# Optimization experiments

Measured on AMD Instinct MI355X. Metric: run time of the kernel, lower is better.

Reference implementation:

```python
import jax, jax.numpy as jnp
import numpy as np

N_TOKENS = 8192
EMBED = 1024
HIDDEN = 4 * EMBED
NUM_EXPERTS = 8


def setup_inputs() -> dict:
    key = jax.random.key(0)
    ks = jax.random.split(key, 10)
    s = 0.02
    return {
        "x": jax.random.normal(ks[0], (N_TOKENS, EMBED), dtype=jnp.float32),
        # Router params
        "Wr1": jax.random.normal(ks[1], (EMBED, EMBED), dtype=jnp.float32) * s,
        "br1": jnp.zeros((EMBED,), dtype=jnp.float32),
        "Wr2": jax.random.normal(ks[2], (EMBED, NUM_EXPERTS), dtype=jnp.float32) * s,
        "br2": jnp.zeros((NUM_EXPERTS,), dtype=jnp.float32),
        # Expert FFN params, stacked over experts
        "W1": jax.random.normal(ks[3], (NUM_EXPERTS, EMBED, HIDDEN), dtype=jnp.float32) * s,
        "b1": jnp.zeros((NUM_EXPERTS, HIDDEN), dtype=jnp.float32),
        "W2": jax.random.normal(ks[4], (NUM_EXPERTS, HIDDEN, EMBED), dtype=jnp.float32) * s,
        "b2": jnp.zeros((NUM_EXPERTS, EMBED), dtype=jnp.float32),
    }


def reference(x, Wr1, br1, Wr2, br2, W1, b1, W2, b2):
    # Router: Linear -> ReLU -> Linear -> softmax over experts -> top-1
    h = jax.nn.relu(x @ Wr1 + br1)                      # [N, E]
    probs = jax.nn.softmax(h @ Wr2 + br2, axis=1)       # [N, num_experts]
    chosen = jnp.argmax(probs, axis=1)                  # [N]

    num_experts = W1.shape[0]
    out = jnp.zeros_like(x)
    # Fixed small loop over experts (structurally distinct weights).
    for e in range(num_experts):
        ffn_e = jax.nn.relu(x @ W1[e] + b1[e]) @ W2[e] + b2[e]  # [N, E]
        out = jnp.where((chosen == e)[:, None], ffn_e, out)
    # Note: original returns raw expert output (no probability weighting).
    return out
```

## Files before the change

kernel.cpp:

```cpp
#include <hip/hip_runtime.h>
#include <stdint.h>

#define N_TOK 8192
#define EMB 1024
#define HID 4096
#define NEXP 8

typedef _Float16 f16x8 __attribute__((ext_vector_type(8)));
typedef _Float16 f16x4 __attribute__((ext_vector_type(4)));
typedef short    s16x8 __attribute__((ext_vector_type(8)));
typedef unsigned short u16x8 __attribute__((ext_vector_type(8)));
typedef float    f32x4 __attribute__((ext_vector_type(4)));

typedef __attribute__((address_space(1))) const void gvoid_t;
typedef __attribute__((address_space(3))) void lvoid_t;

__device__ __forceinline__ void async16(const void* g, void* l) {
  __builtin_amdgcn_global_load_lds((gvoid_t*)g, (lvoid_t*)l, 16, 0, 0);
}

__device__ __forceinline__ unsigned short f2bf(float f) {
  unsigned u = __builtin_bit_cast(unsigned, f);
  u += 0x7fffu + ((u >> 16) & 1u);
  return (unsigned short)(u >> 16);
}

__global__ __launch_bounds__(256) void k_cast_x(const float* __restrict__ x,
    unsigned short* __restrict__ xb, _Float16* __restrict__ xhi, _Float16* __restrict__ xlo) {
  int i = (blockIdx.x * 256 + threadIdx.x) << 2;
  float4 v = *(const float4*)(x + i);
  ushort4 b;
  b.x = f2bf(v.x); b.y = f2bf(v.y); b.z = f2bf(v.z); b.w = f2bf(v.w);
  *(ushort4*)(xb + i) = b;
  float vv[4] = {v.x, v.y, v.z, v.w};
  f16x4 hi, lo;
#pragma unroll
  for (int j = 0; j < 4; j++) {
    _Float16 h = (_Float16)vv[j];
    hi[j] = h;
    lo[j] = (_Float16)(vv[j] - (float)h);
  }
  *(f16x4*)(xhi + i) = hi;
  *(f16x4*)(xlo + i) = lo;
}

__global__ __launch_bounds__(256) void k_trans_wr1(const float* __restrict__ src,
    _Float16* __restrict__ dhi, _Float16* __restrict__ dlo) {
  int nblk = blockIdx.x >> 4, kc = blockIdx.x & 15;
  int n = (nblk << 8) + threadIdx.x;
  int k0 = kc << 6;
  for (int k = k0; k < k0 + 64; k += 8) {
    f16x8 hi, lo;
#pragma unroll
    for (int j = 0; j < 8; j++) {
      float w = src[(size_t)(k + j) * EMB + n] * 256.0f;
      _Float16 h = (_Float16)w;
      hi[j] = h;
      lo[j] = (_Float16)(w - (float)h);
    }
    *(f16x8*)(dhi + (size_t)n * EMB + k) = hi;
    *(f16x8*)(dlo + (size_t)n * EMB + k) = lo;
  }
}

__global__ __launch_bounds__(256) void k_transcast_v2(const float* __restrict__ src,
    unsigned short* __restrict__ dst, int K, int Nn, int ktiles, int ntiles) {
  __shared__ __align__(16) unsigned short lds[256 * 72];
  int b = blockIdx.x;
  int e = b / (ktiles * ntiles);
  int r = b % (ktiles * ntiles);
  int kt = r / ntiles, nt = r % ntiles;
  int k0 = kt << 6, n0 = nt << 8;
  const float* s = src + (size_t)e * K * Nn;
  unsigned short* d = dst + (size_t)e * K * Nn;
  int tid = threadIdx.x;
  const float* scol = s + n0 + tid;
#pragma unroll 4
  for (int k = 0; k < 64; k += 2) {
    float a  = scol[(size_t)(k0 + k) * Nn];
    float bv = scol[(size_t)(k0 + k + 1) * Nn];
    unsigned p = (unsigned)f2bf(a) | ((unsigned)f2bf(bv) << 16);
    *(unsigned*)(lds + tid * 72 + k) = p;
  }
  __syncthreads();
  int c = tid & 7, nl = tid >> 3;
#pragma unroll
  for (int p2 = 0; p2 < 8; p2++) {
    int n = (p2 << 5) + nl;
    u16x8 v = *(const u16x8*)(lds + n * 72 + (c << 3));
    *(u16x8*)(d + (size_t)(n0 + n) * K + k0 + (c << 3)) = v;
  }
}

__global__ __launch_bounds__(256) void k_router_gemm(
    const _Float16* __restrict__ Ah, const _Float16* __restrict__ Al,
    const _Float16* __restrict__ Bh, const _Float16* __restrict__ Bl,
    const float* __restrict__ br1, float* __restrict__ hOut) {
  __shared__ __align__(16) _Float16 sAh[4096], sAl[4096], sBh[4096], sBl[4096];
  const int tid = threadIdx.x, lane = tid & 63, wave = tid >> 6;
  const int m0 = (blockIdx.x >> 3) << 7;
  const int n0 = (blockIdx.x & 7) << 7;
  const int srow = (wave << 5) + (lane >> 2);
  const int scol = (lane & 3) << 3;
  const size_t aBase = (size_t)(m0 + srow) * EMB + scol;
  const size_t bBase = (size_t)(n0 + srow) * EMB + scol;
  _Float16* lAh = sAh + (wave << 10);
  _Float16* lAl = sAl + (wave << 10);
  _Float16* lBh = sBh + (wave << 10);
  _Float16* lBl = sBl + (wave << 10);
  const int q = lane >> 4, c = lane & 15;
  const int msub = (wave & 1) << 6, nsub = (wave >> 1) << 6;
  f32x4 acc[4][4];
#pragma unroll
  for (int i = 0; i < 4; i++)
#pragma unroll
    for (int j = 0; j < 4; j++) acc[i][j] = (f32x4){0.f, 0.f, 0.f, 0.f};

  for (int kk = 0; kk < EMB; kk += 32) {
    async16(Ah + aBase + kk, lAh);
    async16(Ah + aBase + 16 * EMB + kk, lAh + 512);
    async16(Al + aBase + kk, lAl);
    async16(Al + aBase + 16 * EMB + kk, lAl + 512);
    async16(Bh + bBase + kk, lBh);
    async16(Bh + bBase + 16 * EMB + kk, lBh + 512);
    async16(Bl + bBase + kk, lBl);
    async16(Bl + bBase + 16 * EMB + kk, lBl + 512);
    __syncthreads();
    f16x8 fah[4], fal[4], fbh[4], fbl[4];
#pragma unroll
    for (int i = 0; i < 4; i++) {
      int ar = msub + (i << 4) + c;
      int br = nsub + (i << 4) + c;
      fah[i] = *(const f16x8*)(sAh + (ar << 5) + (q << 3));
      fal[i] = *(const f16x8*)(sAl + (ar << 5) + (q << 3));
      fbh[i] = *(const f16x8*)(sBh + (br << 5) + (q << 3));
      fbl[i] = *(const f16x8*)(sBl + (br << 5) + (q << 3));
    }
#pragma unroll
    for (int mi = 0; mi < 4; mi++)
#pragma unroll
      for (int ni = 0; ni < 4; ni++) {
        acc[mi][ni] = __builtin_amdgcn_mfma_f32_16x16x32_f16(fah[mi], fbh[ni], acc[mi][ni], 0, 0, 0);
        acc[mi][ni] = __builtin_amdgcn_mfma_f32_16x16x32_f16(fah[mi], fbl[ni], acc[mi][ni], 0, 0, 0);
        acc[mi][ni] = __builtin_amdgcn_mfma_f32_16x16x32_f16(fal[mi], fbh[ni], acc[mi][ni], 0, 0, 0);
      }
    __syncthreads();
  }
#pragma unroll
  for (int mi = 0; mi < 4; mi++)
#pragma unroll
    for (int ni = 0; ni < 4; ni++) {
      int gn = n0 + nsub + (ni << 4) + c;
      float bias = 256.0f * br1[gn];
#pragma unroll
      for (int i2 = 0; i2 < 4; i2++) {
        int gm = m0 + msub + (mi << 4) + (q << 2) + i2;
        float v = acc[mi][ni][i2] + bias;
        hOut[(size_t)gm * EMB + gn] = v > 0.f ? v : 0.f;
      }
    }
}

__global__ __launch_bounds__(256) void k_logits(const float* __restrict__ h,
    const float* __restrict__ Wr2, const float* __restrict__ br2, int* __restrict__ chosen) {
  __shared__ __align__(16) float sW[EMB * NEXP];
  int tid = threadIdx.x;
  for (int i = tid; i < EMB * NEXP; i += 256) sW[i] = Wr2[i];
  __syncthreads();
  int lane = tid & 63, wave = tid >> 6;
  int t = blockIdx.x * 4 + wave;
  const float* hr = h + (size_t)t * EMB;
  float acc[8] = {0.f, 0.f, 0.f, 0.f, 0.f, 0.f, 0.f, 0.f};
#pragma unroll
  for (int i = 0; i < 16; i++) {
    int k = (i << 6) + lane;
    float v = hr[k];
    float4 w0 = *(const float4*)(sW + (k << 3));
    float4 w1 = *(const float4*)(sW + (k << 3) + 4);
    acc[0] += v * w0.x; acc[1] += v * w0.y; acc[2] += v * w0.z; acc[3] += v * w0.w;
    acc[4] += v * w1.x; acc[5] += v * w1.y; acc[6] += v * w1.z; acc[7] += v * w1.w;
  }
#pragma unroll
  for (int off = 32; off > 0; off >>= 1)
#pragma unroll
    for (int e = 0; e < 8; e++) acc[e] += __shfl_down(acc[e], off);
  if (lane == 0) {
    float best = acc[0] + 256.0f * br2[0];
    int bi = 0;
#pragma unroll
    for (int e = 1; e < 8; e++) {
      float l = acc[e] + 256.0f * br2[e];
      if (l > best) { best = l; bi = e; }
    }
    chosen[t] = bi;
  }
}

__global__ void k_zero(int* meta) { meta[threadIdx.x] = 0; }

__global__ __launch_bounds__(256) void k_hist(const int* __restrict__ chosen, int* meta) {
  int i = blockIdx.x * 256 + threadIdx.x;
  atomicAdd(&meta[chosen[i]], 1);
}

__global__ __launch_bounds__(128) void k_sched(int* meta) {
  __shared__ int cnt[8];
  int tid = threadIdx.x;
  if (tid < 8) cnt[tid] = meta[tid];
  __syncthreads();
  int off[9]; off[0] = 0;
#pragma unroll
  for (int e = 0; e < 8; e++) off[e + 1] = off[e] + cnt[e];
  int ts[9]; ts[0] = 0;
#pragma unroll
  for (int e = 0; e < 8; e++) ts[e + 1] = ts[e] + ((cnt[e] + 127) >> 7);
  int T = ts[8];
  if (tid < 8) meta[16 + tid] = off[tid];
  if (tid == 0) { meta[24] = off[8]; meta[25] = T; }
  if (tid < T) {
    int e = 0;
    while (ts[e + 1] <= tid) e++;
    int m = off[e] + ((tid - ts[e]) << 7);
    int end = off[e + 1];
    meta[32 + tid] = e;
    meta[112 + tid] = m;
    meta[192 + tid] = (m + 128 < end) ? m + 128 : end;
  }
}

__global__ __launch_bounds__(256) void k_scatter(const int* __restrict__ chosen,
                                                 int* meta, int* __restrict__ perm) {
  int i = blockIdx.x * 256 + threadIdx.x;
  int e = chosen[i];
  int pos = meta[16 + e] + atomicAdd(&meta[8 + e], 1);
  perm[pos] = i;
}

__global__ __launch_bounds__(256) void k_ffn1(
    const unsigned short* __restrict__ xb, const unsigned short* __restrict__ w1t,
    const float* __restrict__ b1, const int* __restrict__ perm,
    const int* __restrict__ meta, unsigned short* __restrict__ hidden) {
  const int mt = blockIdx.x >> 5;
  if (mt >= meta[25]) return;
  const int nt = blockIdx.x & 31;
  const int e = meta[32 + mt];
  const int row0 = meta[112 + mt];
  const int rend = meta[192 + mt];
  const int n0 = nt << 7;
  __shared__ __align__(16) unsigned short sA[4096], sB[4096];
  const int tid = threadIdx.x, lane = tid & 63, wave = tid >> 6;
  const int srow = (wave << 5) + (lane >> 2);
  const int scol = (lane & 3) << 3;
  int ra0 = row0 + srow, ra1 = row0 + srow + 16;
  if (ra0 > rend - 1) ra0 = rend - 1;
  if (ra1 > rend - 1) ra1 = rend - 1;
  const int t0 = perm[ra0], t1 = perm[ra1];
  const unsigned short* a0 = xb + (size_t)t0 * EMB + scol;
  const unsigned short* a1 = xb + (size_t)t1 * EMB + scol;
  const unsigned short* bsrc = w1t + (size_t)e * EMB * HID + (size_t)(n0 + srow) * EMB + scol;
  unsigned short* lA = sA + (wave << 10);
  unsigned short* lB = sB + (wave << 10);
  const int q = lane >> 4, c = lane & 15;
  const int msub = (wave & 1) << 6, nsub = (wave >> 1) << 6;
  f32x4 acc[4][4];
#pragma unroll
  for (int i = 0; i < 4; i++)
#pragma unroll
    for (int j = 0; j < 4; j++) acc[i][j] = (f32x4){0.f, 0.f, 0.f, 0.f};

  for (int kk = 0; kk < EMB; kk += 32) {
    async16(a0 + kk, lA);
    async16(a1 + kk, lA + 512);
    async16(bsrc + kk, lB);
    async16(bsrc + 16 * EMB + kk, lB + 512);
    __syncthreads();
    s16x8 fa[4], fb[4];
#pragma unroll
    for (int i = 0; i < 4; i++) {
      fa[i] = *(const s16x8*)(sA + ((msub + (i << 4) + c) << 5) + (q << 3));
      fb[i] = *(const s16x8*)(sB + ((nsub + (i << 4) + c) << 5) + (q << 3));
    }
#pragma unroll
    for (int mi = 0; mi < 4; mi++)
#pragma unroll
      for (int ni = 0; ni < 4; ni++)
        acc[mi][ni] = __builtin_amdgcn_mfma_f32_16x16x32_bf16(fa[mi], fb[ni], acc[mi][ni], 0, 0, 0);
    __syncthreads();
  }
#pragma unroll
  for (int mi = 0; mi < 4; mi++)
#pragma unroll
    for (int ni = 0; ni < 4; ni++) {
      int gn = n0 + nsub + (ni << 4) + c;
      float bias = b1[e * HID + gn];
#pragma unroll
      for (int i2 = 0; i2 < 4; i2++) {
        int rs = row0 + msub + (mi << 4) + (q << 2) + i2;
        if (rs < rend) {
          float v = acc[mi][ni][i2] + bias;
          v = v > 0.f ? v : 0.f;
          hidden[(size_t)rs * HID + gn] = f2bf(v);
        }
      }
    }
}

__global__ __launch_bounds__(256) void k_ffn2(
    const unsigned short* __restrict__ hidden, const unsigned short* __restrict__ w2t,
    const float* __restrict__ b2, const int* __restrict__ perm,
    const int* __restrict__ meta, float* __restrict__ out) {
  const int mt = blockIdx.x >> 3;
  if (mt >= meta[25]) return;
  const int nt = blockIdx.x & 7;
  const int e = meta[32 + mt];
  const int row0 = meta[112 + mt];
  const int rend = meta[192 + mt];
  const int n0 = nt << 7;
  __shared__ __align__(16) unsigned short sA[4096], sB[4096];
  const int tid = threadIdx.x, lane = tid & 63, wave = tid >> 6;
  const int srow = (wave << 5) + (lane >> 2);
  const int scol = (lane & 3) << 3;
  int ra0 = row0 + srow, ra1 = row0 + srow + 16;
  if (ra0 > N_TOK - 1) ra0 = N_TOK - 1;
  if (ra1 > N_TOK - 1) ra1 = N_TOK - 1;
  const unsigned short* a0 = hidden + (size_t)ra0 * HID + scol;
  const unsigned short* a1 = hidden + (size_t)ra1 * HID + scol;
  const unsigned short* bsrc = w2t + (size_t)e * HID * EMB + (size_t)(n0 + srow) * HID + scol;
  unsigned short* lA = sA + (wave << 10);
  unsigned short* lB = sB + (wave << 10);
  const int q = lane >> 4, c = lane & 15;
  const int msub = (wave & 1) << 6, nsub = (wave >> 1) << 6;
  f32x4 acc[4][4];
#pragma unroll
  for (int i = 0; i < 4; i++)
#pragma unroll
    for (int j = 0; j < 4; j++) acc[i][j] = (f32x4){0.f, 0.f, 0.f, 0.f};

  for (int kk = 0; kk < HID; kk += 32) {
    async16(a0 + kk, lA);
    async16(a1 + kk, lA + 512);
    async16(bsrc + kk, lB);
    async16(bsrc + 16 * HID + kk, lB + 512);
    __syncthreads();
    s16x8 fa[4], fb[4];
#pragma unroll
    for (int i = 0; i < 4; i++) {
      fa[i] = *(const s16x8*)(sA + ((msub + (i << 4) + c) << 5) + (q << 3));
      fb[i] = *(const s16x8*)(sB + ((nsub + (i << 4) + c) << 5) + (q << 3));
    }
#pragma unroll
    for (int mi = 0; mi < 4; mi++)
#pragma unroll
      for (int ni = 0; ni < 4; ni++)
        acc[mi][ni] = __builtin_amdgcn_mfma_f32_16x16x32_bf16(fa[mi], fb[ni], acc[mi][ni], 0, 0, 0);
    __syncthreads();
  }
#pragma unroll
  for (int mi = 0; mi < 4; mi++)
#pragma unroll
    for (int ni = 0; ni < 4; ni++) {
      int gn = n0 + nsub + (ni << 4) + c;
      float bias = b2[e * EMB + gn];
#pragma unroll
      for (int i2 = 0; i2 < 4; i2++) {
        int rs = row0 + msub + (mi << 4) + (q << 2) + i2;
        if (rs < rend) {
          int orig = perm[rs];
          out[(size_t)orig * EMB + gn] = acc[mi][ni][i2] + bias;
        }
      }
    }
}

extern "C" void kernel_launch(void* const* d_in, const int* in_sizes, int n_in,
                              void* d_out, int out_size, void* d_ws, size_t ws_size,
                              hipStream_t stream) {
  const float* x   = (const float*)d_in[0];
  const float* Wr1 = (const float*)d_in[1];
  const float* br1 = (const float*)d_in[2];
  const float* Wr2 = (const float*)d_in[3];
  const float* br2 = (const float*)d_in[4];
  const float* W1  = (const float*)d_in[5];
  const float* b1  = (const float*)d_in[6];
  const float* W2  = (const float*)d_in[7];
  const float* b2  = (const float*)d_in[8];
  float* out = (float*)d_out;
  char* ws = (char*)d_ws;

  unsigned short* w1t    = (unsigned short*)(ws + 0);
  unsigned short* w2t    = (unsigned short*)(ws + 67108864);
  unsigned short* xb     = (unsigned short*)(ws + 134217728);
  _Float16*       xhi    = (_Float16*)(ws + 150994944);
  _Float16*       xlo    = (_Float16*)(ws + 167772160);
  _Float16*       whi    = (_Float16*)(ws + 184549376);
  _Float16*       wlo    = (_Float16*)(ws + 186646528);
  float*          hbuf   = (float*)(ws + 188743680);
  unsigned short* hidden = (unsigned short*)(ws + 222298112);
  int*            chosen = (int*)(ws + 289406976);
  int*            perm   = (int*)(ws + 289439744);
  int*            meta   = (int*)(ws + 289472512);

  k_cast_x<<<dim3(8192), dim3(256), 0, stream>>>(x, xb, xhi, xlo);
  k_trans_wr1<<<dim3(64), dim3(256), 0, stream>>>(Wr1, whi, wlo);
  k_transcast_v2<<<dim3(2048), dim3(256), 0, stream>>>(W1, w1t, 1024, 4096, 16, 16);
  k_transcast_v2<<<dim3(2048), dim3(256), 0, stream>>>(W2, w2t, 4096, 1024, 64, 4);
  k_router_gemm<<<dim3(512), dim3(256), 0, stream>>>(xhi, xlo, whi, wlo, br1, hbuf);
  k_logits<<<dim3(2048), dim3(256), 0, stream>>>(hbuf, Wr2, br2, chosen);
  k_zero<<<dim3(1), dim3(256), 0, stream>>>(meta);
  k_hist<<<dim3(32), dim3(256), 0, stream>>>(chosen, meta);
  k_sched<<<dim3(1), dim3(128), 0, stream>>>(meta);
  k_scatter<<<dim3(32), dim3(256), 0, stream>>>(chosen, meta, perm);
  k_ffn1<<<dim3(2304), dim3(256), 0, stream>>>(xb, w1t, b1, perm, meta, hidden);
  k_ffn2<<<dim3(576), dim3(256), 0, stream>>>(hidden, w2t, b2, perm, meta, out);
}
```

Before: 775.7 us.

## Remap GEMM blocks per XCD, change LDS staging layout, split-K ffn2

Block indices in the router GEMM, ffn1 and ffn2 are remapped so that tiles sharing A rows land on the same XCD, which is meant to improve L2 reuse. The LDS staging layout changes so each lane's async 16-byte load goes straight to its MFMA fragment position, giving contiguous, conflict-free fragment reads. ffn2 is split into two K halves to double its block count for occupancy. The second half writes partials into the reused hbuf and a new add kernel sums them, which costs extra traffic on the output tensor and one more launch.

```diff
diff --git a/kernel.cpp b/kernel.cpp
--- a/kernel.cpp
+++ b/kernel.cpp
@@ -98,18 +98,20 @@
     const float* __restrict__ br1, float* __restrict__ hOut) {
   __shared__ __align__(16) _Float16 sAh[4096], sAl[4096], sBh[4096], sBl[4096];
   const int tid = threadIdx.x, lane = tid & 63, wave = tid >> 6;
-  const int m0 = (blockIdx.x >> 3) << 7;
-  const int n0 = (blockIdx.x & 7) << 7;
-  const int srow = (wave << 5) + (lane >> 2);
-  const int scol = (lane & 3) << 3;
-  const size_t aBase = (size_t)(m0 + srow) * EMB + scol;
-  const size_t bBase = (size_t)(n0 + srow) * EMB + scol;
+  const int bid = blockIdx.x;
+  const int xcd = bid & 7, s = bid >> 3;
+  const int m0 = ((xcd << 3) + (s & 7)) << 7;
+  const int n0 = (s >> 3) << 7;
+  const int row16 = lane & 15, kb3 = (lane >> 4) << 3;
+  const size_t aBase = (size_t)(m0 + (wave << 5) + row16) * EMB + kb3;
+  const size_t bBase = (size_t)(n0 + (wave << 5) + row16) * EMB + kb3;
   _Float16* lAh = sAh + (wave << 10);
   _Float16* lAl = sAl + (wave << 10);
   _Float16* lBh = sBh + (wave << 10);
   _Float16* lBl = sBl + (wave << 10);
   const int q = lane >> 4, c = lane & 15;
   const int msub = (wave & 1) << 6, nsub = (wave >> 1) << 6;
+  const int ca = (wave & 1) << 2, cb = (wave >> 1) << 2;
   f32x4 acc[4][4];
 #pragma unroll
   for (int i = 0; i < 4; i++)
@@ -129,12 +131,10 @@
     f16x8 fah[4], fal[4], fbh[4], fbl[4];
 #pragma unroll
     for (int i = 0; i < 4; i++) {
-      int ar = msub + (i << 4) + c;
-      int br = nsub + (i << 4) + c;
-      fah[i] = *(const f16x8*)(sAh + (ar << 5) + (q << 3));
-      fal[i] = *(const f16x8*)(sAl + (ar << 5) + (q << 3));
-      fbh[i] = *(const f16x8*)(sBh + (br << 5) + (q << 3));
-      fbl[i] = *(const f16x8*)(sBl + (br << 5) + (q << 3));
+      fah[i] = *(const f16x8*)(sAh + ((ca + i) << 9) + (lane << 3));
+      fal[i] = *(const f16x8*)(sAl + ((ca + i) << 9) + (lane << 3));
+      fbh[i] = *(const f16x8*)(sBh + ((cb + i) << 9) + (lane << 3));
+      fbl[i] = *(const f16x8*)(sBl + ((cb + i) << 9) + (lane << 3));
     }
 #pragma unroll
     for (int mi = 0; mi < 4; mi++)
@@ -240,28 +240,32 @@
     const unsigned short* __restrict__ xb, const unsigned short* __restrict__ w1t,
     const float* __restrict__ b1, const int* __restrict__ perm,
     const int* __restrict__ meta, unsigned short* __restrict__ hidden) {
-  const int mt = blockIdx.x >> 5;
+  const int bid = blockIdx.x;
+  const int xcd = bid & 7, s = bid >> 3;
+  const int mt = xcd * 9 + (s % 9);
+  const int nt = s / 9;
   if (mt >= meta[25]) return;
-  const int nt = blockIdx.x & 31;
   const int e = meta[32 + mt];
   const int row0 = meta[112 + mt];
   const int rend = meta[192 + mt];
   const int n0 = nt << 7;
   __shared__ __align__(16) unsigned short sA[4096], sB[4096];
   const int tid = threadIdx.x, lane = tid & 63, wave = tid >> 6;
-  const int srow = (wave << 5) + (lane >> 2);
-  const int scol = (lane & 3) << 3;
-  int ra0 = row0 + srow, ra1 = row0 + srow + 16;
-  if (ra0 > rend - 1) ra0 = rend - 1;
-  if (ra1 > rend - 1) ra1 = rend - 1;
-  const int t0 = perm[ra0], t1 = perm[ra1];
-  const unsigned short* a0 = xb + (size_t)t0 * EMB + scol;
-  const unsigned short* a1 = xb + (size_t)t1 * EMB + scol;
-  const unsigned short* bsrc = w1t + (size_t)e * EMB * HID + (size_t)(n0 + srow) * EMB + scol;
+  const int row16 = lane & 15, kb3 = (lane >> 4) << 3;
+  int r0 = row0 + (wave << 5) + row16;
+  int r1 = r0 + 16;
+  if (r0 > rend - 1) r0 = rend - 1;
+  if (r1 > rend - 1) r1 = rend - 1;
+  const int t0 = perm[r0], t1 = perm[r1];
+  const unsigned short* a0 = xb + (size_t)t0 * EMB + kb3;
+  const unsigned short* a1 = xb + (size_t)t1 * EMB + kb3;
+  const unsigned short* bsrc = w1t + (size_t)e * EMB * HID +
+                               (size_t)(n0 + (wave << 5) + row16) * EMB + kb3;
   unsigned short* lA = sA + (wave << 10);
   unsigned short* lB = sB + (wave << 10);
   const int q = lane >> 4, c = lane & 15;
   const int msub = (wave & 1) << 6, nsub = (wave >> 1) << 6;
+  const int ca = (wave & 1) << 2, cb = (wave >> 1) << 2;
   f32x4 acc[4][4];
 #pragma unroll
   for (int i = 0; i < 4; i++)
@@ -277,8 +281,8 @@
     s16x8 fa[4], fb[4];
 #pragma unroll
     for (int i = 0; i < 4; i++) {
-      fa[i] = *(const s16x8*)(sA + ((msub + (i << 4) + c) << 5) + (q << 3));
-      fb[i] = *(const s16x8*)(sB + ((nsub + (i << 4) + c) << 5) + (q << 3));
+      fa[i] = *(const s16x8*)(sA + ((ca + i) << 9) + (lane << 3));
+      fb[i] = *(const s16x8*)(sB + ((cb + i) << 9) + (lane << 3));
     }
 #pragma unroll
     for (int mi = 0; mi < 4; mi++)
@@ -308,35 +312,42 @@
 __global__ __launch_bounds__(256) void k_ffn2(
     const unsigned short* __restrict__ hidden, const unsigned short* __restrict__ w2t,
     const float* __restrict__ b2, const int* __restrict__ perm,
-    const int* __restrict__ meta, float* __restrict__ out) {
-  const int mt = blockIdx.x >> 3;
+    const int* __restrict__ meta, float* __restrict__ out, float* __restrict__ pbuf) {
+  const int bid = blockIdx.x;
+  const int xcd = bid & 7, s = bid >> 3;
+  const int kh = s / 72;
+  const int s2 = s % 72;
+  const int mt = xcd * 9 + (s2 >> 3);
+  const int nt = s2 & 7;
   if (mt >= meta[25]) return;
-  const int nt = blockIdx.x & 7;
   const int e = meta[32 + mt];
   const int row0 = meta[112 + mt];
   const int rend = meta[192 + mt];
   const int n0 = nt << 7;
+  const int kbase = kh << 11;
   __shared__ __align__(16) unsigned short sA[4096], sB[4096];
   const int tid = threadIdx.x, lane = tid & 63, wave = tid >> 6;
-  const int srow = (wave << 5) + (lane >> 2);
-  const int scol = (lane & 3) << 3;
-  int ra0 = row0 + srow, ra1 = row0 + srow + 16;
-  if (ra0 > N_TOK - 1) ra0 = N_TOK - 1;
-  if (ra1 > N_TOK - 1) ra1 = N_TOK - 1;
-  const unsigned short* a0 = hidden + (size_t)ra0 * HID + scol;
-  const unsigned short* a1 = hidden + (size_t)ra1 * HID + scol;
-  const unsigned short* bsrc = w2t + (size_t)e * HID * EMB + (size_t)(n0 + srow) * HID + scol;
+  const int row16 = lane & 15, kb3 = (lane >> 4) << 3;
+  int r0 = row0 + (wave << 5) + row16;
+  int r1 = r0 + 16;
+  if (r0 > N_TOK - 1) r0 = N_TOK - 1;
+  if (r1 > N_TOK - 1) r1 = N_TOK - 1;
+  const unsigned short* a0 = hidden + (size_t)r0 * HID + kbase + kb3;
+  const unsigned short* a1 = hidden + (size_t)r1 * HID + kbase + kb3;
+  const unsigned short* bsrc = w2t + (size_t)e * HID * EMB +
+                               (size_t)(n0 + (wave << 5) + row16) * HID + kbase + kb3;
   unsigned short* lA = sA + (wave << 10);
   unsigned short* lB = sB + (wave << 10);
   const int q = lane >> 4, c = lane & 15;
   const int msub = (wave & 1) << 6, nsub = (wave >> 1) << 6;
+  const int ca = (wave & 1) << 2, cb = (wave >> 1) << 2;
   f32x4 acc[4][4];
 #pragma unroll
   for (int i = 0; i < 4; i++)
 #pragma unroll
     for (int j = 0; j < 4; j++) acc[i][j] = (f32x4){0.f, 0.f, 0.f, 0.f};
 
-  for (int kk = 0; kk < HID; kk += 32) {
+  for (int kk = 0; kk < 2048; kk += 32) {
     async16(a0 + kk, lA);
     async16(a1 + kk, lA + 512);
     async16(bsrc + kk, lB);
@@ -345,8 +356,8 @@
     s16x8 fa[4], fb[4];
 #pragma unroll
     for (int i = 0; i < 4; i++) {
-      fa[i] = *(const s16x8*)(sA + ((msub + (i << 4) + c) << 5) + (q << 3));
-      fb[i] = *(const s16x8*)(sB + ((nsub + (i << 4) + c) << 5) + (q << 3));
+      fa[i] = *(const s16x8*)(sA + ((ca + i) << 9) + (lane << 3));
+      fb[i] = *(const s16x8*)(sB + ((cb + i) << 9) + (lane << 3));
     }
 #pragma unroll
     for (int mi = 0; mi < 4; mi++)
@@ -355,21 +366,31 @@
         acc[mi][ni] = __builtin_amdgcn_mfma_f32_16x16x32_bf16(fa[mi], fb[ni], acc[mi][ni], 0, 0, 0);
     __syncthreads();
   }
+  float* dst = kh ? pbuf : out;
 #pragma unroll
   for (int mi = 0; mi < 4; mi++)
 #pragma unroll
     for (int ni = 0; ni < 4; ni++) {
       int gn = n0 + nsub + (ni << 4) + c;
-      float bias = b2[e * EMB + gn];
+      float bias = kh ? 0.f : b2[e * EMB + gn];
 #pragma unroll
       for (int i2 = 0; i2 < 4; i2++) {
         int rs = row0 + msub + (mi << 4) + (q << 2) + i2;
         if (rs < rend) {
           int orig = perm[rs];
-          out[(size_t)orig * EMB + gn] = acc[mi][ni][i2] + bias;
+          dst[(size_t)orig * EMB + gn] = acc[mi][ni][i2] + bias;
         }
       }
     }
+}
+
+__global__ __launch_bounds__(256) void k_add(float* __restrict__ out,
+                                             const float* __restrict__ pbuf) {
+  int i = (blockIdx.x * 256 + threadIdx.x) << 2;
+  float4 a = *(const float4*)(out + i);
+  float4 b = *(const float4*)(pbuf + i);
+  a.x += b.x; a.y += b.y; a.z += b.z; a.w += b.w;
+  *(float4*)(out + i) = a;
 }
 
 extern "C" void kernel_launch(void* const* d_in, const int* in_sizes, int n_in,
@@ -411,5 +432,6 @@
   k_sched<<<dim3(1), dim3(128), 0, stream>>>(meta);
   k_scatter<<<dim3(32), dim3(256), 0, stream>>>(chosen, meta, perm);
   k_ffn1<<<dim3(2304), dim3(256), 0, stream>>>(xb, w1t, b1, perm, meta, hidden);
-  k_ffn2<<<dim3(576), dim3(256), 0, stream>>>(hidden, w2t, b2, perm, meta, out);
-}
+  k_ffn2<<<dim3(1152), dim3(256), 0, stream>>>(hidden, w2t, b2, perm, meta, out, hbuf);
+  k_add<<<dim3(8192), dim3(256), 0, stream>>>(out, hbuf);
+}
```

Measured after the change: 902.6 us. +16.4%, slower.

## Split-K the expert FFN2 GEMM in two halves and fold zeroing into logits

Applied to the files above, without the earlier changes.

FFN2 now splits its 4096-long reduction into two halves, doubling the grid to 1152 blocks. The first half writes to the output with bias and the second writes a partial sum into the reused router hbuf. A new elementwise kernel then adds the two results. Separately, the meta-zeroing launch is folded into block 0 of k_logits to drop one kernel launch. The aim is better CU occupancy for FFN2, whose 576-block grid underfills the GPU, at the cost of an extra 32MB read-modify-write pass. The meta zeroing happens inside k_logits while other blocks run, which is safe only because k_hist runs later.

```diff
diff --git a/kernel.cpp b/kernel.cpp
--- a/kernel.cpp
+++ b/kernel.cpp
@@ -162,9 +162,13 @@
 }
 
 __global__ __launch_bounds__(256) void k_logits(const float* __restrict__ h,
-    const float* __restrict__ Wr2, const float* __restrict__ br2, int* __restrict__ chosen) {
+    const float* __restrict__ Wr2, const float* __restrict__ br2, int* __restrict__ chosen,
+    int* __restrict__ meta) {
   __shared__ __align__(16) float sW[EMB * NEXP];
   int tid = threadIdx.x;
+  if (blockIdx.x == 0) {
+    for (int i = tid; i < 264; i += 256) meta[i] = 0;
+  }
   for (int i = tid; i < EMB * NEXP; i += 256) sW[i] = Wr2[i];
   __syncthreads();
   int lane = tid & 63, wave = tid >> 6;
@@ -195,8 +199,6 @@
     chosen[t] = bi;
   }
 }
-
-__global__ void k_zero(int* meta) { meta[threadIdx.x] = 0; }
 
 __global__ __launch_bounds__(256) void k_hist(const int* __restrict__ chosen, int* meta) {
   int i = blockIdx.x * 256 + threadIdx.x;
@@ -251,13 +253,14 @@
   const int tid = threadIdx.x, lane = tid & 63, wave = tid >> 6;
   const int srow = (wave << 5) + (lane >> 2);
   const int scol = (lane & 3) << 3;
-  int ra0 = row0 + srow, ra1 = row0 + srow + 16;
-  if (ra0 > rend - 1) ra0 = rend - 1;
-  if (ra1 > rend - 1) ra1 = rend - 1;
-  const int t0 = perm[ra0], t1 = perm[ra1];
+  int r0 = row0 + srow, r1 = r0 + 16;
+  if (r0 > rend - 1) r0 = rend - 1;
+  if (r1 > rend - 1) r1 = rend - 1;
+  const int t0 = perm[r0], t1 = perm[r1];
   const unsigned short* a0 = xb + (size_t)t0 * EMB + scol;
   const unsigned short* a1 = xb + (size_t)t1 * EMB + scol;
-  const unsigned short* bsrc = w1t + (size_t)e * EMB * HID + (size_t)(n0 + srow) * EMB + scol;
+  const unsigned short* bsrc = w1t + (size_t)e * EMB * HID +
+                               (size_t)(n0 + srow) * EMB + scol;
   unsigned short* lA = sA + (wave << 10);
   unsigned short* lB = sB + (wave << 10);
   const int q = lane >> 4, c = lane & 15;
@@ -308,24 +311,28 @@
 __global__ __launch_bounds__(256) void k_ffn2(
     const unsigned short* __restrict__ hidden, const unsigned short* __restrict__ w2t,
     const float* __restrict__ b2, const int* __restrict__ perm,
-    const int* __restrict__ meta, float* __restrict__ out) {
-  const int mt = blockIdx.x >> 3;
+    const int* __restrict__ meta, float* __restrict__ out, float* __restrict__ pbuf) {
+  const int mt = blockIdx.x >> 4;
   if (mt >= meta[25]) return;
-  const int nt = blockIdx.x & 7;
+  const int r = blockIdx.x & 15;
+  const int kh = r >> 3;
+  const int nt = r & 7;
   const int e = meta[32 + mt];
   const int row0 = meta[112 + mt];
   const int rend = meta[192 + mt];
   const int n0 = nt << 7;
+  const int kbase = kh << 11;
   __shared__ __align__(16) unsigned short sA[4096], sB[4096];
   const int tid = threadIdx.x, lane = tid & 63, wave = tid >> 6;
   const int srow = (wave << 5) + (lane >> 2);
   const int scol = (lane & 3) << 3;
-  int ra0 = row0 + srow, ra1 = row0 + srow + 16;
-  if (ra0 > N_TOK - 1) ra0 = N_TOK - 1;
-  if (ra1 > N_TOK - 1) ra1 = N_TOK - 1;
-  const unsigned short* a0 = hidden + (size_t)ra0 * HID + scol;
-  const unsigned short* a1 = hidden + (size_t)ra1 * HID + scol;
-  const unsigned short* bsrc = w2t + (size_t)e * HID * EMB + (size_t)(n0 + srow) * HID + scol;
+  int r0 = row0 + srow, r1 = r0 + 16;
+  if (r0 > N_TOK - 1) r0 = N_TOK - 1;
+  if (r1 > N_TOK - 1) r1 = N_TOK - 1;
+  const unsigned short* a0 = hidden + (size_t)r0 * HID + kbase + scol;
+  const unsigned short* a1 = hidden + (size_t)r1 * HID + kbase + scol;
+  const unsigned short* bsrc = w2t + (size_t)e * HID * EMB +
+                               (size_t)(n0 + srow) * HID + kbase + scol;
   unsigned short* lA = sA + (wave << 10);
   unsigned short* lB = sB + (wave << 10);
   const int q = lane >> 4, c = lane & 15;
@@ -336,7 +343,7 @@
 #pragma unroll
     for (int j = 0; j < 4; j++) acc[i][j] = (f32x4){0.f, 0.f, 0.f, 0.f};
 
-  for (int kk = 0; kk < HID; kk += 32) {
+  for (int kk = 0; kk < 2048; kk += 32) {
     async16(a0 + kk, lA);
     async16(a1 + kk, lA + 512);
     async16(bsrc + kk, lB);
@@ -355,21 +362,31 @@
         acc[mi][ni] = __builtin_amdgcn_mfma_f32_16x16x32_bf16(fa[mi], fb[ni], acc[mi][ni], 0, 0, 0);
     __syncthreads();
   }
+  float* dst = kh ? pbuf : out;
 #pragma unroll
   for (int mi = 0; mi < 4; mi++)
 #pragma unroll
     for (int ni = 0; ni < 4; ni++) {
       int gn = n0 + nsub + (ni << 4) + c;
-      float bias = b2[e * EMB + gn];
+      float bias = kh ? 0.f : b2[e * EMB + gn];
 #pragma unroll
       for (int i2 = 0; i2 < 4; i2++) {
         int rs = row0 + msub + (mi << 4) + (q << 2) + i2;
         if (rs < rend) {
           int orig = perm[rs];
-          out[(size_t)orig * EMB + gn] = acc[mi][ni][i2] + bias;
+          dst[(size_t)orig * EMB + gn] = acc[mi][ni][i2] + bias;
         }
       }
     }
+}
+
+__global__ __launch_bounds__(256) void k_add(float* __restrict__ out,
+                                             const float* __restrict__ pbuf) {
+  int i = (blockIdx.x * 256 + threadIdx.x) << 2;
+  float4 a = *(const float4*)(out + i);
+  float4 b = *(const float4*)(pbuf + i);
+  a.x += b.x; a.y += b.y; a.z += b.z; a.w += b.w;
+  *(float4*)(out + i) = a;
 }
 
 extern "C" void kernel_launch(void* const* d_in, const int* in_sizes, int n_in,
@@ -405,11 +422,11 @@
   k_transcast_v2<<<dim3(2048), dim3(256), 0, stream>>>(W1, w1t, 1024, 4096, 16, 16);
   k_transcast_v2<<<dim3(2048), dim3(256), 0, stream>>>(W2, w2t, 4096, 1024, 64, 4);
   k_router_gemm<<<dim3(512), dim3(256), 0, stream>>>(xhi, xlo, whi, wlo, br1, hbuf);
-  k_logits<<<dim3(2048), dim3(256), 0, stream>>>(hbuf, Wr2, br2, chosen);
-  k_zero<<<dim3(1), dim3(256), 0, stream>>>(meta);
+  k_logits<<<dim3(2048), dim3(256), 0, stream>>>(hbuf, Wr2, br2, chosen, meta);
   k_hist<<<dim3(32), dim3(256), 0, stream>>>(chosen, meta);
   k_sched<<<dim3(1), dim3(128), 0, stream>>>(meta);
   k_scatter<<<dim3(32), dim3(256), 0, stream>>>(chosen, meta, perm);
   k_ffn1<<<dim3(2304), dim3(256), 0, stream>>>(xb, w1t, b1, perm, meta, hidden);
-  k_ffn2<<<dim3(576), dim3(256), 0, stream>>>(hidden, w2t, b2, perm, meta, out);
-}
+  k_ffn2<<<dim3(1152), dim3(256), 0, stream>>>(hidden, w2t, b2, perm, meta, out, hbuf);
+  k_add<<<dim3(8192), dim3(256), 0, stream>>>(out, hbuf);
+}
```

After: 788.0 us. Within noise of the previous version (+1.6%).
